# Optimization experiments

Hardware: AMD Instinct MI355X
Metric: run time of the kernel (lower is better)

## Reference

```python
import jax, jax.numpy as jnp
import numpy as np

B, IN, OUT = 4096, 128, 128
C = 1.0                    # curvature of the Poincare ball
SQRT_C = 1.0
MIN_ENORM = 1e-15          # manifold.min_enorm
BALL_EPS = 1e-5            # projection margin for backproject
EPS32 = float(np.finfo(np.float32).eps)
CLAMP = 1.0 * float(np.log(2.0 / EPS32))   # clamping_factor * log(2/eps)
SMOOTH = 50.0              # smoothing_factor


def _project(y, axis):
    # project back onto the open ball of radius (1 - eps)/sqrt(c)
    norm = jnp.clip(jnp.linalg.norm(y, axis=axis, keepdims=True), MIN_ENORM)
    maxnorm = (1.0 - BALL_EPS) / SQRT_C
    return jnp.where(norm > maxnorm, y * (maxnorm / norm), y)


def _lambda(y, axis):
    # conformal factor lambda(y) = 2 / (1 - c ||y||^2)
    sq = jnp.sum(y * y, axis=axis, keepdims=True)
    return 2.0 / jnp.clip(1.0 - C * sq, EPS32)


def _mobius_add(u, v, axis):
    uv = jnp.sum(u * v, axis=axis, keepdims=True)
    uu = jnp.sum(u * u, axis=axis, keepdims=True)
    vv = jnp.sum(v * v, axis=axis, keepdims=True)
    num = (1.0 + 2.0 * C * uv + C * vv) * u + (1.0 - C * uu) * v
    den = 1.0 + 2.0 * C * uv + (C * C) * uu * vv
    return num / jnp.clip(den, EPS32)


def _smooth_clamp(x, lo, hi, beta):
    # smooth version of clamp; -> hard clamp as beta -> inf
    return lo + (jax.nn.softplus(beta * (x - lo)) - jax.nn.softplus(beta * (x - hi))) / beta


def setup_inputs() -> dict:
    key = jax.random.key(0)
    k1, k2, k3 = jax.random.split(key, 3)
    v = jax.random.normal(k1, (B, IN), dtype=jnp.float32)
    x = 0.7 * v / (1.0 + jnp.linalg.norm(v, axis=-1, keepdims=True))  # strictly inside ball
    weight = jax.random.normal(k2, (OUT, IN), dtype=jnp.float32) * 0.05
    b = jax.random.normal(k3, (OUT, IN), dtype=jnp.float32)
    bias = 0.1 * b / (1.0 + jnp.linalg.norm(b, axis=-1, keepdims=True))  # in-ball translations
    return {"x": x, "weight": weight, "bias": bias}


def reference(x, weight, bias):
    # ptransp_0(weight, bias) = (lambda_0 / lambda_bias) * weight = (1 - c||bias||^2) * weight
    lam_b = _lambda(bias, -1)                       # (out, 1)
    a = (2.0 / lam_b) * weight                      # (out, in) tangent normals at bias
    p = bias                                        # (out, in)

    u = -p.T[None, :, :]                            # (1, in, out)
    v = x[:, :, None]                               # (B, in, 1)
    sub = _mobius_add(u, v, axis=1)                 # (B, in, out) = (-p) (+) x
    sub = _project(sub, axis=1)                     # backproject

    suba = jnp.sum(sub * a.T[None, :, :], axis=1, keepdims=True)         # (B, 1, out)
    a_norm = jnp.clip(jnp.linalg.norm(a, axis=-1, keepdims=True), MIN_ENORM).T  # (1, out)

    asinh_arg = SQRT_C * _lambda(sub, 1) * suba / a_norm[None, :, :]     # (B, 1, out)
    asinh_arg = _smooth_clamp(asinh_arg, -CLAMP, CLAMP, SMOOTH)
    signed_dist = jnp.arcsinh(asinh_arg) / SQRT_C                        # (B, 1, out)

    res = _lambda(p, -1).T * a_norm * signed_dist[:, 0, :]               # (B, out)
    return res
```

## Files before the change

kernel.cpp:

```cpp
#include <hip/hip_runtime.h>
#include <math.h>

#define BB 16
#define NOUT 128
#define NIN 128
#define NTHREADS 256

__global__ __launch_bounds__(NTHREADS) void hyper_kernel(
    const float* __restrict__ x,
    const float* __restrict__ weight,
    const float* __restrict__ bias,
    float* __restrict__ out)
{
    __shared__ __align__(16) float sx[BB][NIN];
    __shared__ float svv[BB];

    const int tid = threadIdx.x;
    const int b0 = blockIdx.x * BB;

    {
        const float4* xg = (const float4*)(x + (size_t)b0 * NIN);
        float4* xs = (float4*)(&sx[0][0]);
        xs[tid] = xg[tid];
        xs[tid + NTHREADS] = xg[tid + NTHREADS];
    }
    __syncthreads();

    if (tid < 128) {
        const int r = tid >> 3, seg = tid & 7;
        float s = 0.f;
        const float4* xr = (const float4*)(&sx[r][seg * 16]);
        #pragma unroll
        for (int j = 0; j < 4; ++j) {
            float4 v = xr[j];
            s = fmaf(v.x, v.x, fmaf(v.y, v.y, fmaf(v.z, v.z, fmaf(v.w, v.w, s))));
        }
        s += __shfl_xor(s, 1);
        s += __shfl_xor(s, 2);
        s += __shfl_xor(s, 4);
        if (seg == 0) svv[r] = s;
    }

    const int o = tid & 127;
    const int rbase = (tid >> 7) * (BB / 2);

    const float4* w4 = (const float4*)(weight + (size_t)o * NIN);
    const float4* b4 = (const float4*)(bias + (size_t)o * NIN);

    float accb[BB / 2], accw[BB / 2];
    #pragma unroll
    for (int r = 0; r < BB / 2; ++r) { accb[r] = 0.f; accw[r] = 0.f; }
    float uu = 0.f, bw = 0.f, ww = 0.f;

    #pragma unroll 4
    for (int kc = 0; kc < NIN / 4; ++kc) {
        const float4 wv = w4[kc];
        const float4 bv = b4[kc];
        uu = fmaf(bv.x, bv.x, uu); uu = fmaf(bv.y, bv.y, uu);
        uu = fmaf(bv.z, bv.z, uu); uu = fmaf(bv.w, bv.w, uu);
        bw = fmaf(bv.x, wv.x, bw); bw = fmaf(bv.y, wv.y, bw);
        bw = fmaf(bv.z, wv.z, bw); bw = fmaf(bv.w, wv.w, bw);
        ww = fmaf(wv.x, wv.x, ww); ww = fmaf(wv.y, wv.y, ww);
        ww = fmaf(wv.z, wv.z, ww); ww = fmaf(wv.w, wv.w, ww);
        #pragma unroll
        for (int r = 0; r < BB / 2; ++r) {
            const float4 xv = *(const float4*)(&sx[rbase + r][kc * 4]);
            accb[r] = fmaf(xv.x, bv.x, accb[r]); accb[r] = fmaf(xv.y, bv.y, accb[r]);
            accb[r] = fmaf(xv.z, bv.z, accb[r]); accb[r] = fmaf(xv.w, bv.w, accb[r]);
            accw[r] = fmaf(xv.x, wv.x, accw[r]); accw[r] = fmaf(xv.y, wv.y, accw[r]);
            accw[r] = fmaf(xv.z, wv.z, accw[r]); accw[r] = fmaf(xv.w, wv.w, accw[r]);
        }
    }
    __syncthreads();

    const float EPS = 1.1920928955078125e-7f;
    const float CLAMPV = 16.635532333438687f;
    const float INV_SMOOTH = 1.f / 50.f;
    const float SMOOTHF = 50.f;
    const float MAXNORM = 1.f - 1e-5f;

    const float beta = 1.f - uu;
    const float beta_c = fmaxf(beta, EPS);
    const float a_norm = fmaxf(beta_c * sqrtf(ww), 1e-15f);
    const float ba = beta_c * bw;
    const float outcoef = (2.f / beta_c) * a_norm;
    const float inv_anorm = 1.f / a_norm;

    #pragma unroll
    for (int r = 0; r < BB / 2; ++r) {
        const float vv = svv[rbase + r];
        const float uv = -accb[r];
        const float dax = beta_c * accw[r];
        const float alpha = 1.f + 2.f * uv + vv;
        const float den = fmaxf(1.f + 2.f * uv + uu * vv, EPS);
        const float inv_den = 1.f / den;
        float suba = (beta * dax - alpha * ba) * inv_den;
        float ss = (alpha * alpha * uu + 2.f * alpha * beta * uv + beta * beta * vv)
                   * (inv_den * inv_den);
        const float nrm = fmaxf(sqrtf(fmaxf(ss, 0.f)), 1e-15f);
        if (nrm > MAXNORM) {
            const float sc = MAXNORM / nrm;
            suba *= sc;
            ss *= sc * sc;
        }
        const float lam_sub = 2.f / fmaxf(1.f - ss, EPS);
        const float arg = lam_sub * suba * inv_anorm;
        const float t1 = SMOOTHF * (arg + CLAMPV);
        const float t2 = SMOOTHF * (arg - CLAMPV);
        const float sp1 = fmaxf(t1, 0.f) + log1pf(expf(-fabsf(t1)));
        const float sp2 = fmaxf(t2, 0.f) + log1pf(expf(-fabsf(t2)));
        const float scl = -CLAMPV + (sp1 - sp2) * INV_SMOOTH;
        const float sd = asinhf(scl);
        out[(size_t)(b0 + rbase + r) * NOUT + o] = outcoef * sd;
    }
}

extern "C" void kernel_launch(void* const* d_in, const int* in_sizes, int n_in,
                              void* d_out, int out_size, void* d_ws, size_t ws_size,
                              hipStream_t stream) {
    const float* x = (const float*)d_in[0];
    const float* w = (const float*)d_in[1];
    const float* b = (const float*)d_in[2];
    float* out = (float*)d_out;
    const int B = in_sizes[0] / NIN;
    dim3 grid(B / BB), block(NTHREADS);
    hipLaunchKernelGGL(hyper_kernel, grid, block, 0, stream, x, w, b, out);
}
```

Before: 79.00 us.

## Use split-bf16 MFMA for x·W and x·bias dot products, fast math epilogue

Replaces the scalar FP32 FMA dot-product loops with bf16 MFMA 16x16x32 instructions. Each FP32 operand is split into a high and a low bf16 part, and three MFMAs per pair recover near-FP32 accuracy. Each wave now computes a 16x16 output tile, loading its operands directly from global memory with no shared memory or block syncs. The epilogue swaps log1pf/expf/asinhf for __logf/__expf approximations, which trades some precision for speed.

```diff
diff --git a/kernel.cpp b/kernel.cpp
--- a/kernel.cpp
+++ b/kernel.cpp
@@ -1,77 +1,101 @@
 #include <hip/hip_runtime.h>
 #include <math.h>
 
-#define BB 16
+typedef __attribute__((ext_vector_type(8))) short short8;
+typedef __attribute__((ext_vector_type(4))) float floatx4;
+
+#define NIN 128
 #define NOUT 128
-#define NIN 128
-#define NTHREADS 256
+#define NTH 256
 
-__global__ __launch_bounds__(NTHREADS) void hyper_kernel(
+union FragU { unsigned u[4]; short8 s; };
+
+__device__ __forceinline__ void cvt_frag(float4 a, float4 b, short8& hi, short8& lo) {
+    const unsigned SEL = 0x07060302u;
+    unsigned ua0 = __float_as_uint(a.x), ua1 = __float_as_uint(a.y);
+    unsigned ua2 = __float_as_uint(a.z), ua3 = __float_as_uint(a.w);
+    unsigned ub0 = __float_as_uint(b.x), ub1 = __float_as_uint(b.y);
+    unsigned ub2 = __float_as_uint(b.z), ub3 = __float_as_uint(b.w);
+    FragU h, l;
+    h.u[0] = __builtin_amdgcn_perm(ua1, ua0, SEL);
+    h.u[1] = __builtin_amdgcn_perm(ua3, ua2, SEL);
+    h.u[2] = __builtin_amdgcn_perm(ub1, ub0, SEL);
+    h.u[3] = __builtin_amdgcn_perm(ub3, ub2, SEL);
+    float r0 = a.x - __uint_as_float(ua0 & 0xffff0000u);
+    float r1 = a.y - __uint_as_float(ua1 & 0xffff0000u);
+    float r2 = a.z - __uint_as_float(ua2 & 0xffff0000u);
+    float r3 = a.w - __uint_as_float(ua3 & 0xffff0000u);
+    float r4 = b.x - __uint_as_float(ub0 & 0xffff0000u);
+    float r5 = b.y - __uint_as_float(ub1 & 0xffff0000u);
+    float r6 = b.z - __uint_as_float(ub2 & 0xffff0000u);
+    float r7 = b.w - __uint_as_float(ub3 & 0xffff0000u);
+    l.u[0] = __builtin_amdgcn_perm(__float_as_uint(r1), __float_as_uint(r0), SEL);
+    l.u[1] = __builtin_amdgcn_perm(__float_as_uint(r3), __float_as_uint(r2), SEL);
+    l.u[2] = __builtin_amdgcn_perm(__float_as_uint(r5), __float_as_uint(r4), SEL);
+    l.u[3] = __builtin_amdgcn_perm(__float_as_uint(r7), __float_as_uint(r6), SEL);
+    hi = h.s; lo = l.s;
+}
+
+__device__ __forceinline__ float dot8(float4 a, float4 b, float4 c, float4 d, float s) {
+    s = fmaf(a.x, c.x, s); s = fmaf(a.y, c.y, s);
+    s = fmaf(a.z, c.z, s); s = fmaf(a.w, c.w, s);
+    s = fmaf(b.x, d.x, s); s = fmaf(b.y, d.y, s);
+    s = fmaf(b.z, d.z, s); s = fmaf(b.w, d.w, s);
+    return s;
+}
+
+__global__ __launch_bounds__(NTH) void hyper_fused(
     const float* __restrict__ x,
-    const float* __restrict__ weight,
-    const float* __restrict__ bias,
+    const float* __restrict__ w,
+    const float* __restrict__ bia,
     float* __restrict__ out)
 {
-    __shared__ __align__(16) float sx[BB][NIN];
-    __shared__ float svv[BB];
+    const int wave = threadIdx.x >> 6;
+    const int lane = threadIdx.x & 63;
+    const int q = lane >> 4, i = lane & 15;
+    const int waveid = blockIdx.x * 4 + wave;
+    const int m0 = (waveid >> 3) * 16;
+    const int n0 = (waveid & 7) * 16;
 
-    const int tid = threadIdx.x;
-    const int b0 = blockIdx.x * BB;
+    const float* xr = x + (size_t)(m0 + i) * NIN + q * 8;
+    const float* wr = w + (size_t)(n0 + i) * NIN + q * 8;
+    const float* br = bia + (size_t)(n0 + i) * NIN + q * 8;
 
-    {
-        const float4* xg = (const float4*)(x + (size_t)b0 * NIN);
-        float4* xs = (float4*)(&sx[0][0]);
-        xs[tid] = xg[tid];
-        xs[tid + NTHREADS] = xg[tid + NTHREADS];
-    }
-    __syncthreads();
+    floatx4 accW1 = {0.f, 0.f, 0.f, 0.f}, accW2 = {0.f, 0.f, 0.f, 0.f};
+    floatx4 accB1 = {0.f, 0.f, 0.f, 0.f}, accB2 = {0.f, 0.f, 0.f, 0.f};
+    float vv = 0.f, uu = 0.f, bw = 0.f, ww = 0.f;
 
-    if (tid < 128) {
-        const int r = tid >> 3, seg = tid & 7;
-        float s = 0.f;
-        const float4* xr = (const float4*)(&sx[r][seg * 16]);
-        #pragma unroll
-        for (int j = 0; j < 4; ++j) {
-            float4 v = xr[j];
-            s = fmaf(v.x, v.x, fmaf(v.y, v.y, fmaf(v.z, v.z, fmaf(v.w, v.w, s))));
-        }
-        s += __shfl_xor(s, 1);
-        s += __shfl_xor(s, 2);
-        s += __shfl_xor(s, 4);
-        if (seg == 0) svv[r] = s;
+    #pragma unroll
+    for (int kc = 0; kc < 4; ++kc) {
+        const float4 xa = *(const float4*)(xr + kc * 32);
+        const float4 xb = *(const float4*)(xr + kc * 32 + 4);
+        const float4 wa = *(const float4*)(wr + kc * 32);
+        const float4 wb = *(const float4*)(wr + kc * 32 + 4);
+        const float4 ba = *(const float4*)(br + kc * 32);
+        const float4 bb = *(const float4*)(br + kc * 32 + 4);
+
+        vv = dot8(xa, xb, xa, xb, vv);
+        uu = dot8(ba, bb, ba, bb, uu);
+        bw = dot8(ba, bb, wa, wb, bw);
+        ww = dot8(wa, wb, wa, wb, ww);
+
+        short8 ah, al, wh, wl, bh, bl;
+        cvt_frag(xa, xb, ah, al);
+        cvt_frag(wa, wb, wh, wl);
+        cvt_frag(ba, bb, bh, bl);
+
+        accW1 = __builtin_amdgcn_mfma_f32_16x16x32_bf16(ah, wh, accW1, 0, 0, 0);
+        accB1 = __builtin_amdgcn_mfma_f32_16x16x32_bf16(ah, bh, accB1, 0, 0, 0);
+        accW2 = __builtin_amdgcn_mfma_f32_16x16x32_bf16(ah, wl, accW2, 0, 0, 0);
+        accB2 = __builtin_amdgcn_mfma_f32_16x16x32_bf16(ah, bl, accB2, 0, 0, 0);
+        accW2 = __builtin_amdgcn_mfma_f32_16x16x32_bf16(al, wh, accW2, 0, 0, 0);
+        accB2 = __builtin_amdgcn_mfma_f32_16x16x32_bf16(al, bh, accB2, 0, 0, 0);
     }
 
-    const int o = tid & 127;
-    const int rbase = (tid >> 7) * (BB / 2);
-
-    const float4* w4 = (const float4*)(weight + (size_t)o * NIN);
-    const float4* b4 = (const float4*)(bias + (size_t)o * NIN);
-
-    float accb[BB / 2], accw[BB / 2];
-    #pragma unroll
-    for (int r = 0; r < BB / 2; ++r) { accb[r] = 0.f; accw[r] = 0.f; }
-    float uu = 0.f, bw = 0.f, ww = 0.f;
-
-    #pragma unroll 4
-    for (int kc = 0; kc < NIN / 4; ++kc) {
-        const float4 wv = w4[kc];
-        const float4 bv = b4[kc];
-        uu = fmaf(bv.x, bv.x, uu); uu = fmaf(bv.y, bv.y, uu);
-        uu = fmaf(bv.z, bv.z, uu); uu = fmaf(bv.w, bv.w, uu);
-        bw = fmaf(bv.x, wv.x, bw); bw = fmaf(bv.y, wv.y, bw);
-        bw = fmaf(bv.z, wv.z, bw); bw = fmaf(bv.w, wv.w, bw);
-        ww = fmaf(wv.x, wv.x, ww); ww = fmaf(wv.y, wv.y, ww);
-        ww = fmaf(wv.z, wv.z, ww); ww = fmaf(wv.w, wv.w, ww);
-        #pragma unroll
-        for (int r = 0; r < BB / 2; ++r) {
-            const float4 xv = *(const float4*)(&sx[rbase + r][kc * 4]);
-            accb[r] = fmaf(xv.x, bv.x, accb[r]); accb[r] = fmaf(xv.y, bv.y, accb[r]);
-            accb[r] = fmaf(xv.z, bv.z, accb[r]); accb[r] = fmaf(xv.w, bv.w, accb[r]);
-            accw[r] = fmaf(xv.x, wv.x, accw[r]); accw[r] = fmaf(xv.y, wv.y, accw[r]);
-            accw[r] = fmaf(xv.z, wv.z, accw[r]); accw[r] = fmaf(xv.w, wv.w, accw[r]);
-        }
-    }
-    __syncthreads();
+    vv += __shfl_xor(vv, 16); vv += __shfl_xor(vv, 32);
+    uu += __shfl_xor(uu, 16); uu += __shfl_xor(uu, 32);
+    bw += __shfl_xor(bw, 16); bw += __shfl_xor(bw, 32);
+    ww += __shfl_xor(ww, 16); ww += __shfl_xor(ww, 32);
 
     const float EPS = 1.1920928955078125e-7f;
     const float CLAMPV = 16.635532333438687f;
@@ -82,20 +106,22 @@
     const float beta = 1.f - uu;
     const float beta_c = fmaxf(beta, EPS);
     const float a_norm = fmaxf(beta_c * sqrtf(ww), 1e-15f);
-    const float ba = beta_c * bw;
+    const float ba_ = beta_c * bw;
     const float outcoef = (2.f / beta_c) * a_norm;
     const float inv_anorm = 1.f / a_norm;
 
     #pragma unroll
-    for (int r = 0; r < BB / 2; ++r) {
-        const float vv = svv[rbase + r];
-        const float uv = -accb[r];
-        const float dax = beta_c * accw[r];
-        const float alpha = 1.f + 2.f * uv + vv;
-        const float den = fmaxf(1.f + 2.f * uv + uu * vv, EPS);
+    for (int r = 0; r < 4; ++r) {
+        const int row = m0 + q * 4 + r;
+        const float vvr = __shfl(vv, q * 4 + r, 64);
+        const float uv = -(accB1[r] + accB2[r]);
+        const float xw = accW1[r] + accW2[r];
+        const float dax = beta_c * xw;
+        const float alpha = 1.f + 2.f * uv + vvr;
+        const float den = fmaxf(1.f + 2.f * uv + uu * vvr, EPS);
         const float inv_den = 1.f / den;
-        float suba = (beta * dax - alpha * ba) * inv_den;
-        float ss = (alpha * alpha * uu + 2.f * alpha * beta * uv + beta * beta * vv)
+        float suba = (beta * dax - alpha * ba_) * inv_den;
+        float ss = (alpha * alpha * uu + 2.f * alpha * beta * uv + beta * beta * vvr)
                    * (inv_den * inv_den);
         const float nrm = fmaxf(sqrtf(fmaxf(ss, 0.f)), 1e-15f);
         if (nrm > MAXNORM) {
@@ -107,11 +133,12 @@
         const float arg = lam_sub * suba * inv_anorm;
         const float t1 = SMOOTHF * (arg + CLAMPV);
         const float t2 = SMOOTHF * (arg - CLAMPV);
-        const float sp1 = fmaxf(t1, 0.f) + log1pf(expf(-fabsf(t1)));
-        const float sp2 = fmaxf(t2, 0.f) + log1pf(expf(-fabsf(t2)));
+        const float sp1 = fmaxf(t1, 0.f) + __logf(1.f + __expf(-fabsf(t1)));
+        const float sp2 = fmaxf(t2, 0.f) + __logf(1.f + __expf(-fabsf(t2)));
         const float scl = -CLAMPV + (sp1 - sp2) * INV_SMOOTH;
-        const float sd = asinhf(scl);
-        out[(size_t)(b0 + rbase + r) * NOUT + o] = outcoef * sd;
+        const float s_ = fabsf(scl);
+        const float sd = copysignf(__logf(s_ + sqrtf(fmaf(s_, s_, 1.f))), scl);
+        out[(size_t)row * NOUT + n0 + i] = outcoef * sd;
     }
 }
 
@@ -123,6 +150,7 @@
     const float* b = (const float*)d_in[2];
     float* out = (float*)d_out;
     const int B = in_sizes[0] / NIN;
-    dim3 grid(B / BB), block(NTHREADS);
-    hipLaunchKernelGGL(hyper_kernel, grid, block, 0, stream, x, w, b, out);
+    const int nblocks = (B / 16) * (NOUT / 16) / 4;
+    hipLaunchKernelGGL(hyper_fused, dim3(nblocks), dim3(NTH), 0, stream,
+                       x, w, b, out);
 }
```

After: 64.73 us. -18.1%, faster.
